# Performance work log

Hardware: AMD Instinct MI355X
Metric: run time of the kernel (lower is better)

## Reference

```python
import jax, jax.numpy as jnp
import numpy as np
from jax.scipy.special import xlogy

LAMBDA_XM = 0.05
LAMBDA_SEG2D = 1.0
BN_EPS = 1e-5


def setup_inputs() -> dict:
    key = jax.random.key(0)
    ks = jax.random.split(key, 40)
    S, N, Nv, B, Np, M, H, C, MID = 2, 240000, 80000, 2, 120000, 30000, 64, 20, 16
    Nimg = B * M
    f = lambda i, shape, s=0.05: jax.random.normal(ks[i], shape, jnp.float32) * s
    inp = {
        'img_feat': f(0, (S, Nimg, H), 1.0),
        'pts_feat': f(1, (S, Nv, H), 1.0),
        'coors_inv': jax.random.randint(ks[2], (S, N), 0, Nv),
        'labels': jax.random.randint(ks[3], (N,), 0, C),
        'img_label': jax.random.randint(ks[4], (Nimg,), 0, C),
        'p2img_idx': jax.random.randint(ks[5], (B, M), 0, Np),
        # multihead 3d classifiers (per scale): Linear(H,128)-ReLU-Linear(128,C)
        'w3a': f(6, (S, H, 128)), 'b3a': jnp.zeros((S, 128)),
        'w3b': f(7, (S, 128, C)), 'b3b': jnp.zeros((S, C)),
        # multihead fuse classifiers
        'wfa': f(8, (S, H, 128)), 'bfa': jnp.zeros((S, 128)),
        'wfb': f(9, (S, 128, C)), 'bfb': jnp.zeros((S, C)),
        # attention: fc1(H->H//4), fc2(H->H//4), fc3(H//2->2), conv1/conv2 (1x1 -> linear) + BN
        'fc1w': f(10, (S, H, MID)), 'fc1b': jnp.zeros((S, MID)),
        'fc2w': f(11, (S, H, MID)), 'fc2b': jnp.zeros((S, MID)),
        'fc3w': f(12, (S, 2 * MID, 2)), 'fc3b': jnp.zeros((S, 2)),
        'c1w': f(13, (S, H, H)), 'c1b': jnp.zeros((S, H)),
        'bn1g': jnp.ones((S, H)), 'bn1b': jnp.zeros((S, H)),
        'c2w': f(14, (S, H, H)), 'c2b': jnp.zeros((S, H)),
        'bn2g': jnp.ones((S, H)), 'bn2b': jnp.zeros((S, H)),
        # final classifier Linear(S*H,128)-ReLU-Linear(128,C)
        'clw1': f(15, (S * H, 128)), 'clb1': jnp.zeros((128,)),
        'clw2': f(16, (128, C)), 'clb2': jnp.zeros((C,)),
    }
    return inp


def _mlp2(x, w1, b1, w2, b2):
    return jax.nn.relu(x @ w1 + b1) @ w2 + b2


def _ce(logits, lab):
    logp = jax.nn.log_softmax(logits, -1)
    return -jnp.take_along_axis(logp, lab[:, None], axis=1).mean()


def _lovasz(probs, lab):
    # lovasz-softmax over all classes, averaged over present classes
    C = probs.shape[1]
    fg = jax.nn.one_hot(lab, C, dtype=probs.dtype)  # [N,C]
    errors = jnp.abs(fg - probs)

    def per_class(err_c, fg_c):
        order = jnp.argsort(-err_c)
        e = err_c[order]
        f = fg_c[order]
        gts = f.sum()
        inter = gts - jnp.cumsum(f)
        union = gts + jnp.cumsum(1.0 - f)
        jac = 1.0 - inter / union
        jac = jnp.concatenate([jac[:1], jac[1:] - jac[:-1]])
        return jnp.dot(e, jac)

    losses = jax.vmap(per_class)(errors.T, fg.T)  # [C]
    present = (fg.sum(0) > 0).astype(probs.dtype)
    return jnp.sum(losses * present) / jnp.maximum(present.sum(), 1.0)


def _seg_loss(logits, lab):
    return _ce(logits, lab) + _lovasz(jax.nn.softmax(logits, -1), lab)


def _convbn_relu(x, cw, cb, g, b):
    # 1x1 Conv1d == per-point linear; BN (training-mode batch stats over points)
    y = x @ cw + cb
    mu = y.mean(0)
    var = y.var(0)
    return jax.nn.relu((y - mu) * jax.lax.rsqrt(var + BN_EPS) * g + b)


def reference(img_feat, pts_feat, coors_inv, labels, img_label, p2img_idx,
              w3a, b3a, w3b, b3b, wfa, bfa, wfb, bfb,
              fc1w, fc1b, fc2w, fc2b, fc3w, fc3b,
              c1w, c1b, bn1g, bn1b, c2w, c2b, bn2g, bn2b,
              clw1, clb1, clw2, clb2):
    S, Nv, H = pts_feat.shape
    C = w3b.shape[-1]
    B, M = p2img_idx.shape
    N = labels.shape[0]
    Np = N // B
    # p2img_mapping: per-batch gather composed to one global gather (batch blocks are contiguous/equal)
    gidx = (jnp.arange(B)[:, None] * Np + p2img_idx).reshape(-1)  # [Nimg]

    loss = jnp.float32(0.0)
    feats = []
    for s in range(S):
        pred3d = _mlp2(pts_feat[s], w3a[s], b3a[s], w3b[s], b3b[s])  # [Nv,C]
        # voxelize_labels: majority vote per voxel (== unique+scatter_max count argmax)
        counts = jnp.zeros((Nv, C), jnp.float32).at[coors_inv[s], labels].add(1.0)
        vox_lab = jnp.argmax(counts, axis=1)  # [Nv]
        # gather voxel feats/preds to image-projected points (fused gather)
        idx = coors_inv[s][gidx]  # [Nimg]
        p = pts_feat[s][idx]      # [Nimg,H] pseudo feats
        pts_pred = pred3d[idx]    # [Nimg,C]
        v = img_feat[s]           # [Nimg,H] valid (image) feats
        # Attention fusion
        w = jax.nn.sigmoid(
            jnp.concatenate([p @ fc1w[s] + fc1b[s], v @ fc2w[s] + fc2b[s]], -1) @ fc3w[s] + fc3b[s])  # [Nimg,2]
        fuse = (_convbn_relu(p, c1w[s], c1b[s], bn1g[s], bn1b[s]) * w[:, 0:1]
                + _convbn_relu(v, c2w[s], c2b[s], bn2g[s], bn2b[s]) * w[:, 1:2])
        feats.append(fuse)
        fuse_pred = _mlp2(fuse, wfa[s], bfa[s], wfb[s], bfb[s])
        loss = loss + _seg_loss(pred3d, vox_lab)
        loss = loss + _seg_loss(fuse_pred, img_label) * LAMBDA_SEG2D / S
        # F.kl_div(log_softmax(pts_pred), softmax(fuse_pred)), reduction='mean' over all elements
        pf = jax.nn.softmax(fuse_pred, -1)
        kl = jnp.mean(xlogy(pf, pf) - pf * jax.nn.log_softmax(pts_pred, -1))
        loss = loss + kl * LAMBDA_XM / S
    img_logits = _mlp2(jnp.concatenate(feats, -1), clw1, clb1, clw2, clb2)
    loss = loss + _seg_loss(img_logits, img_label)
    return loss
```

## Files before the change

kernel.cpp:

```cpp
#include <hip/hip_runtime.h>
#include <stdint.h>

static constexpr int NV   = 80000;
static constexpr int NPT  = 240000;
static constexpr int NIMG = 60000;
static constexpr int Hh   = 64;
static constexpr int Cc   = 20;
static constexpr int NPp  = 120000;
static constexpr int Mm   = 30000;
static constexpr int NB     = 8192;
static constexpr int NCH    = 16;
static constexpr int NBLK_GA  = (NIMG + 63) / 64;
static constexpr int NBLK_MLP = NV / 64;
static constexpr int NBLK_CNT = (NPT + 255) / 256;
static constexpr int NBLK_FILL_NV = (NV + 255) / 256;
static constexpr int NBLK_FILL_NI = (NIMG + 255) / 256;
static constexpr int NBLK_HIST = Cc * NCH;
static constexpr int NBLK_GATH = 2 * NIMG * 8 / 256;
static constexpr int NBLK_P3G  = (2 * NIMG + 255) / 256;
#define BN_EPS 1e-5f

using bf16x8 = __attribute__((ext_vector_type(8))) short;
using f32x4  = __attribute__((ext_vector_type(4))) float;

__device__ __forceinline__ float waveReduce(float v) {
  #pragma unroll
  for (int o = 32; o > 0; o >>= 1) v += __shfl_down(v, o);
  return v;
}
__device__ __forceinline__ short f2bf(float f) {
  uint32_t u = __float_as_uint(f);
  return (short)((u + 0x7FFFu + ((u >> 16) & 1u)) >> 16);
}
__device__ __forceinline__ float bf2f(uint32_t h) { return __uint_as_float(h << 16); }
__device__ __forceinline__ uint32_t pk2(float a, float b) {
  return ((uint32_t)(uint16_t)f2bf(a)) | ((uint32_t)(uint16_t)f2bf(b) << 16);
}

struct PackDesc { const float* src; short* dst; int K, Nr, nt; };
struct PackArgs { PackDesc d[14]; };

__global__ void __launch_bounds__(256)
k_pack_zero(PackArgs pa,
            const float* __restrict__ fc1w, const float* __restrict__ fc1b,
            const float* __restrict__ fc2w, const float* __restrict__ fc2b,
            const float* __restrict__ fc3w, const float* __restrict__ fc3b,
            float* __restrict__ attEffs,
            uint4* __restrict__ zb, int zq,
            const int* __restrict__ ci0, const int* __restrict__ ci1,
            const int* __restrict__ p2img,
            int* __restrict__ idx0, int* __restrict__ idx1,
            const float* __restrict__ pts, uint16_t* __restrict__ pgath) {
  int bid = blockIdx.x;
  if (bid >= 384) {
    int g = (bid - 384) * 256 + threadIdx.x;
    int row = g >> 3, q = g & 7;
    int r = (row >= NIMG) ? row - NIMG : row;
    int s1 = (row >= NIMG) ? 1 : 0;
    const int* ci = s1 ? ci1 : ci0;
    int b = (r >= Mm) ? 1 : 0;
    int id = ci[b * NPp + p2img[r]];
    if (q == 0) { if (s1) idx1[r] = id; else idx0[r] = id; }
    const float* src = pts + (size_t)s1 * NV * 64 + (size_t)id * 64 + q * 8;
    float4 a = *(const float4*)src;
    float4 c = *(const float4*)(src + 4);
    uint4 o;
    o.x = pk2(a.x, a.y); o.y = pk2(a.z, a.w);
    o.z = pk2(c.x, c.y); o.w = pk2(c.z, c.w);
    *(uint4*)(pgath + (size_t)row * 64 + q * 8) = o;
    return;
  }
  if (bid >= 128) {
    const uint4 z = make_uint4(0u, 0u, 0u, 0u);
    int i = (bid - 128) * 256 + threadIdx.x;
    for (; i < zq; i += 256 * 256) zb[i] = z;
    return;
  }
  const int stride = 128 * 256;
  for (int di = 0; di < 14; di++) {
    const float* src = pa.d[di].src;
    short* dst = pa.d[di].dst;
    int K = pa.d[di].K, Nr = pa.d[di].Nr, ntiles = pa.d[di].nt;
    int total = (K / 32) * ntiles * 512;
    for (int idx = bid * 256 + threadIdx.x; idx < total; idx += stride) {
      int j = idx & 7, lane = (idx >> 3) & 63, tile = idx >> 9;
      int nt = tile % ntiles, kt = tile / ntiles;
      int k = kt * 32 + (lane >> 4) * 8 + j;
      int n = nt * 16 + (lane & 15);
      float v = (n < Nr) ? src[(size_t)k * Nr + n] : 0.f;
      dst[idx] = f2bf(v);
    }
  }
  if (bid < 2 && threadIdx.x < 64) {
    int s = bid, t = threadIdx.x;
    const float* f1w = fc1w + s * 64 * 16; const float* f1b = fc1b + s * 16;
    const float* f2w = fc2w + s * 64 * 16; const float* f2b = fc2b + s * 16;
    const float* f3w = fc3w + s * 64;      const float* f3b = fc3b + s * 2;
    float* aE = attEffs + s * 320;
    float p0 = 0.f, p1 = 0.f, v0 = 0.f, v1 = 0.f;
    #pragma unroll
    for (int j = 0; j < 16; j++) {
      p0 = fmaf(f1w[t * 16 + j], f3w[j * 2], p0);
      p1 = fmaf(f1w[t * 16 + j], f3w[j * 2 + 1], p1);
      v0 = fmaf(f2w[t * 16 + j], f3w[(16 + j) * 2], v0);
      v1 = fmaf(f2w[t * 16 + j], f3w[(16 + j) * 2 + 1], v1);
    }
    aE[t * 2] = p0; aE[t * 2 + 1] = p1;
    aE[128 + t * 2] = v0; aE[128 + t * 2 + 1] = v1;
    if (t == 0) {
      float b0 = f3b[0], b1 = f3b[1];
      for (int j = 0; j < 16; j++) {
        b0 += f1b[j] * f3w[j * 2] + f2b[j] * f3w[(16 + j) * 2];
        b1 += f1b[j] * f3w[j * 2 + 1] + f2b[j] * f3w[(16 + j) * 2 + 1];
      }
      aE[256] = b0; aE[257] = b1;
    }
  }
}

__device__ void scanbin_body(const unsigned long long* __restrict__ H64,
                             int n, int call, float* __restrict__ lossesC5,
                             int* __restrict__ gts5, int cls) {
  __shared__ int sWC[4], sWF[4];
  __shared__ float sRedF[4];
  int t = threadIdx.x;
  int lane = t & 63, w = t >> 6;
  const uint4* Hv = (const uint4*)(H64 + (size_t)cls * NB + (size_t)t * 32);
  int locC = 0, locF = 0;
  #pragma unroll
  for (int i = 0; i < 16; i++) {
    uint4 u = Hv[i];
    locF += (int)(u.x + u.z);
    locC += (int)(u.y + u.w);
  }
  int sc = locC, sf = locF;
  #pragma unroll
  for (int o = 1; o < 64; o <<= 1) {
    int a = __shfl_up(sc, o);
    int b = __shfl_up(sf, o);
    if (lane >= o) { sc += a; sf += b; }
  }
  if (lane == 63) { sWC[w] = sc; sWF[w] = sf; }
  __syncthreads();
  int offC = 0, offF = 0, Ftot = 0;
  #pragma unroll
  for (int ww = 0; ww < 4; ww++) {
    int fc = sWF[ww];
    Ftot += fc;
    if (ww < w) { offC += sWC[ww]; offF += fc; }
  }
  int runC = offC + sc - locC;
  int runF = offF + sf - locF;
  float gts = (float)Ftot;
  float contrib = 0.f;
  #pragma unroll
  for (int i = 0; i < 16; i++) {
    uint4 u = Hv[i];
    #pragma unroll
    for (int j = 0; j < 2; j++) {
      int cnt = (int)(j ? u.w : u.y), fgc = (int)(j ? u.z : u.x);
      runC += cnt; runF += fgc;
      if (cnt > 0 && Ftot > 0) {
        float r0 = (float)(n - runC);
        float F0 = (float)(Ftot - runF);
        float r1 = r0 + (float)cnt;
        float F1 = F0 + (float)fgc;
        float emean = __uint_as_float((uint32_t)(t * 32 + i * 2 + j) << 17);
        contrib += emean * (r1 / (gts + r1 - F1) - r0 / (gts + r0 - F0));
      }
    }
  }
  contrib = waveReduce(contrib);
  if (lane == 0) sRedF[w] = contrib;
  __syncthreads();
  if (t == 0) {
    lossesC5[call * 32 + cls] = (Ftot > 0) ? (sRedF[0] + sRedF[1] + sRedF[2] + sRedF[3]) : 0.f;
    gts5[call * 32 + cls] = Ftot;
  }
}

__device__ void tile_loss(const float* __restrict__ sL, int r0, int rows, int n,
                          const int* __restrict__ lab, uint16_t* __restrict__ E,
                          float ceScale, float* __restrict__ lossAcc) {
  int t = threadIdx.x;
  if (t < 64) {
    float total = 0.f;
    int gr = r0 + t;
    if (gr < rows) {
      const float* l = sL + t * 21;
      float m = l[0];
      #pragma unroll
      for (int c = 1; c < Cc; c++) m = fmaxf(m, l[c]);
      float ex[Cc]; float se = 0.f;
      #pragma unroll
      for (int c = 0; c < Cc; c++) { ex[c] = expf(l[c] - m); se += ex[c]; }
      float inv = 1.f / se;
      float lse = logf(se);
      int lb = lab[gr];
      total = -(l[lb] - m - lse) * ceScale;
      #pragma unroll
      for (int c = 0; c < Cc; c++) {
        float prob = ex[c] * inv;
        int fg = (c == lb) ? 1 : 0;
        float err = fg ? (1.f - prob) : prob;
        err = fmaxf(err, 0.f);
        uint32_t key = __float_as_uint(err) >> 17;
        E[(size_t)c * n + gr] = (uint16_t)((key << 1) | (uint32_t)fg);
      }
    }
    total = waveReduce(total);
    if (t == 0) atomicAdd(lossAcc, total);
  }
}

template<int D, bool TO_LDS>
__device__ __forceinline__ void mfma_mlp_core(const short* sXb, short* sH, float* sL,
    int r0, int rows,
    const short* __restrict__ pw1, const float* __restrict__ B1,
    const short* __restrict__ pw2, const float* __restrict__ B2,
    float* __restrict__ Out) {
  constexpr int LDB = D + 8;
  constexpr int KT1 = D / 32;
  const int t = threadIdx.x;
  const int lane = t & 63, w = t >> 6;
  const int m = lane & 15, quad = lane >> 4;
  const int rowA = 16 * w + m;
  bf16x8 a1[KT1];
  #pragma unroll
  for (int kt = 0; kt < KT1; kt++)
    a1[kt] = *(const bf16x8*)(sXb + rowA * LDB + kt * 32 + quad * 8);
  __syncthreads();
  const bf16x8* b1 = (const bf16x8*)pw1;
  #pragma unroll
  for (int nt = 0; nt < 8; nt++) {
    f32x4 c = {0.f, 0.f, 0.f, 0.f};
    #pragma unroll
    for (int kt = 0; kt < KT1; kt++)
      c = __builtin_amdgcn_mfma_f32_16x16x32_bf16(a1[kt], b1[(kt * 8 + nt) * 64 + lane], c, 0, 0, 0);
    int col = nt * 16 + m;
    float bc = B1[col];
    #pragma unroll
    for (int reg = 0; reg < 4; reg++)
      sH[(16 * w + quad * 4 + reg) * 136 + col] = f2bf(fmaxf(c[reg] + bc, 0.f));
  }
  __syncthreads();
  bf16x8 a2[4];
  #pragma unroll
  for (int kt = 0; kt < 4; kt++)
    a2[kt] = *(const bf16x8*)(sH + rowA * 136 + kt * 32 + quad * 8);
  if (TO_LDS) __syncthreads();
  const bf16x8* b2 = (const bf16x8*)pw2;
  #pragma unroll
  for (int nt = 0; nt < 2; nt++) {
    f32x4 c = {0.f, 0.f, 0.f, 0.f};
    #pragma unroll
    for (int kt = 0; kt < 4; kt++)
      c = __builtin_amdgcn_mfma_f32_16x16x32_bf16(a2[kt], b2[(kt * 2 + nt) * 64 + lane], c, 0, 0, 0);
    int col = nt * 16 + m;
    if (col < Cc) {
      float bc = B2[col];
      #pragma unroll
      for (int reg = 0; reg < 4; reg++) {
        int rr = 16 * w + quad * 4 + reg;
        if (TO_LDS) {
          sL[rr * 21 + col] = c[reg] + bc;
        } else {
          int gr = r0 + rr;
          if (gr < rows) Out[(size_t)gr * Cc + col] = c[reg] + bc;
        }
      }
    }
  }
}

__device__ void mlp64_body(int bid0, const float* __restrict__ X,
    const short* __restrict__ pw1, const float* __restrict__ B1,
    const short* __restrict__ pw2, const float* __restrict__ B2,
    float* __restrict__ Out, int rows, char* smem) {
  short* buf = (short*)smem;
  int t = threadIdx.x, r0 = bid0 * 64;
  for (int i = t; i < 1024; i += 256) {
    int r = i >> 4, k4 = (i & 15) * 4;
    int gr = r0 + r;
    float4 v = (gr < rows) ? *(const float4*)(X + (size_t)gr * 64 + k4)
                           : make_float4(0.f, 0.f, 0.f, 0.f);
    uint2 p; p.x = pk2(v.x, v.y); p.y = pk2(v.z, v.w);
    *(uint2*)(buf + r * 72 + k4) = p;
  }
  __syncthreads();
  mfma_mlp_core<64, false>(buf, buf, nullptr, r0, rows, pw1, B1, pw2, B2, Out);
}

__device__ void mlp128_loss_body(int bid0, const uint16_t* __restrict__ Xh,
    const short* __restrict__ pw1, const float* __restrict__ B1,
    const short* __restrict__ pw2, const float* __restrict__ B2,
    const int* __restrict__ lab, uint16_t* __restrict__ E, float ce,
    float* __restrict__ lossAcc, char* smem) {
  short* buf = (short*)smem;
  int t = threadIdx.x, r0 = bid0 * 64;
  for (int i = t; i < 2048; i += 256) {
    int r = i >> 5, k4 = (i & 31) * 4;
    int gr = r0 + r;
    uint2 p = (gr < NIMG) ? *(const uint2*)(Xh + (size_t)gr * 128 + k4) : make_uint2(0u, 0u);
    *(uint2*)(buf + r * 136 + k4) = p;
  }
  __syncthreads();
  mfma_mlp_core<128, true>(buf, buf, (float*)buf, r0, NIMG, pw1, B1, pw2, B2, nullptr);
  __syncthreads();
  tile_loss((float*)buf, r0, NIMG, NIMG, lab, E, ce, lossAcc);
}

__device__ void cnt_body(int bid0, const int* __restrict__ ci, const int* __restrict__ labels,
                         int* __restrict__ counts) {
  int i = bid0 * 256 + threadIdx.x;
  if (i < NPT) atomicAdd(&counts[(size_t)ci[i] * Cc + labels[i]], 1);
}

__device__ void colred_body(int bid0, const float* __restrict__ partials,
                            float* __restrict__ red64) {
  int t = threadIdx.x, j = bid0;
  float v = 0.f;
  for (int b = j; b < NBLK_GA; b += 64) v += partials[(size_t)b * 256 + t];
  red64[j * 256 + t] = v;
}

__device__ void p3gath_body(int bid0, const float* __restrict__ pred3d0,
                            const float* __restrict__ pred3d1,
                            const int* __restrict__ idx0, const int* __restrict__ idx1,
                            float* __restrict__ p3g0, float* __restrict__ p3g1) {
  int row = bid0 * 256 + threadIdx.x;
  if (row >= 2 * NIMG) return;
  int s1 = (row >= NIMG) ? 1 : 0;
  int r = s1 ? row - NIMG : row;
  const float* pred = s1 ? pred3d1 : pred3d0;
  float* dst = (s1 ? p3g1 : p3g0) + (size_t)r * Cc;
  const float* src = pred + (size_t)(s1 ? idx1[r] : idx0[r]) * Cc;
  #pragma unroll
  for (int c = 0; c < Cc; c += 2) {
    uint2 v = *(const uint2*)(src + c);
    *(uint2*)(dst + c) = v;
  }
}

__device__ void fill_body(int bid0, const float* __restrict__ logits,
                          const int* __restrict__ lab, const int* __restrict__ vcnt,
                          int n, uint16_t* __restrict__ E,
                          float ceScale, float* __restrict__ lossAcc,
                          const float* __restrict__ p3g, float klScale) {
  int i = bid0 * 256 + threadIdx.x;
  float total = 0.f;
  if (i < n) {
    int lb;
    if (vcnt) {
      const int* crow = vcnt + (size_t)i * Cc;
      int best = crow[0], arg = 0;
      #pragma unroll
      for (int k = 1; k < Cc; k++) {
        int ck = crow[k];
        if (ck > best) { best = ck; arg = k; }
      }
      lb = arg;
    } else {
      lb = lab[i];
    }
    const float* l = logits + (size_t)i * Cc;
    float m = l[0];
    #pragma unroll
    for (int c = 1; c < Cc; c++) m = fmaxf(m, l[c]);
    float ex[Cc]; float se = 0.f;
    #pragma unroll
    for (int c = 0; c < Cc; c++) { ex[c] = expf(l[c] - m); se += ex[c]; }
    float inv = 1.f / se;
    float lse = logf(se);
    total = -(l[lb] - m - lse) * ceScale;
    #pragma unroll
    for (int c = 0; c < Cc; c++) {
      float prob = ex[c] * inv;
      int fg = (c == lb) ? 1 : 0;
      float err = fg ? (1.f - prob) : prob;
      err = fmaxf(err, 0.f);
      uint32_t key = __float_as_uint(err) >> 17;
      E[(size_t)c * n + i] = (uint16_t)((key << 1) | (uint32_t)fg);
    }
    if (p3g) {
      const float* q = p3g + (size_t)i * Cc;
      float mq = q[0];
      #pragma unroll
      for (int c = 1; c < Cc; c++) mq = fmaxf(mq, q[c]);
      float sq = 0.f;
      #pragma unroll
      for (int c = 0; c < Cc; c++) sq += expf(q[c] - mq);
      float lsq = logf(sq);
      float kl = 0.f;
      #pragma unroll
      for (int c = 0; c < Cc; c++) {
        float lf = l[c] - m - lse;
        float pf = ex[c] * inv;
        float lq = q[c] - mq - lsq;
        kl += pf * (lf - lq);
      }
      total += kl * klScale;
    }
  }
  total = waveReduce(total);
  __shared__ float sh[4];
  int lane = threadIdx.x & 63, w = threadIdx.x >> 6;
  if (lane == 0) sh[w] = total;
  __syncthreads();
  if (threadIdx.x == 0) atomicAdd(lossAcc, sh[0] + sh[1] + sh[2] + sh[3]);
}

__device__ void hist_body(int bid0, const uint16_t* __restrict__ E, int n,
                          unsigned long long* __restrict__ H64, char* smem) {
  uint32_t* lcf = (uint32_t*)smem;
  int t = threadIdx.x;
  int cls = bid0 / NCH, ch = bid0 - cls * NCH;
  int CHsz = (n + NCH - 1) / NCH;
  int i0 = ch * CHsz;
  int i1 = min(n, i0 + CHsz);
  for (int b = t; b < NB; b += 256) lcf[b] = 0u;
  __syncthreads();
  const uint16_t* Ec = E + (size_t)cls * n;
  for (int i = i0 + t; i < i1; i += 256) {
    uint32_t p = Ec[i];
    atomicAdd(&lcf[p >> 1], 0x10000u | (p & 1u));
  }
  __syncthreads();
  unsigned long long* Hc = H64 + (size_t)cls * NB;
  for (int b = t; b < NB; b += 256) {
    uint32_t v = lcf[b];
    if (v)
      atomicAdd(&Hc[b], ((unsigned long long)(v >> 16) << 32) | (v & 0xFFFFu));
  }
}

__device__ void gatt_body(int bid0, const uint16_t* __restrict__ pg,
                          const float* __restrict__ img,
                          const short* __restrict__ pc1, const float* __restrict__ c1b,
                          const short* __restrict__ pc2, const float* __restrict__ c2b,
                          const float* __restrict__ attEff,
                          uint16_t* __restrict__ y1, uint16_t* __restrict__ y2,
                          float* __restrict__ attw, float* __restrict__ partials,
                          char* smem) {
  short* sP = (short*)smem;
  short* sV = (short*)(smem + 9216);
  float* sAtt  = (float*)(smem + 18432);
  float* sStat = (float*)smem;
  int t = threadIdx.x;
  int r0 = bid0 * 64;
  for (int i = t; i < 512; i += 256) {
    int r = i >> 3, q = i & 7;
    int gr = r0 + r;
    uint4 pv = make_uint4(0u, 0u, 0u, 0u);
    if (gr < NIMG) pv = *(const uint4*)(pg + (size_t)gr * 64 + q * 8);
    *(uint4*)(sP + r * 72 + q * 8) = pv;
  }
  for (int i = t; i < 1024; i += 256) {
    int r = i >> 4, q = i & 15;
    int gr = r0 + r;
    float4 vv = make_float4(0.f, 0.f, 0.f, 0.f);
    if (gr < NIMG) vv = *(const float4*)(img + (size_t)gr * 64 + q * 4);
    uint2 qv;
    qv.x = pk2(vv.x, vv.y); qv.y = pk2(vv.z, vv.w);
    *(uint2*)(sV + r * 72 + q * 4) = qv;
  }
  __syncthreads();
  {
    int r = t & 63, qq = t >> 6;
    const float* aP = attEff;
    const float* aV = attEff + 128;
    float l0 = 0.f, l1 = 0.f;
    for (int k = qq * 16; k < qq * 16 + 16; k += 4) {
      uint2 up = *(const uint2*)(sP + r * 72 + k);
      uint2 uv = *(const uint2*)(sV + r * 72 + k);
      float p0 = bf2f(up.x & 0xffff), p1 = bf2f(up.x >> 16);
      float p2 = bf2f(up.y & 0xffff), p3 = bf2f(up.y >> 16);
      float v0 = bf2f(uv.x & 0xffff), v1 = bf2f(uv.x >> 16);
      float v2 = bf2f(uv.y & 0xffff), v3 = bf2f(uv.y >> 16);
      float4 wa = *(const float4*)(aP + 2 * k);
      float4 wb = *(const float4*)(aP + 2 * k + 4);
      l0 += p0 * wa.x + p1 * wa.z + p2 * wb.x + p3 * wb.z;
      l1 += p0 * wa.y + p1 * wa.w + p2 * wb.y + p3 * wb.w;
      float4 ua = *(const float4*)(aV + 2 * k);
      float4 ub = *(const float4*)(aV + 2 * k + 4);
      l0 += v0 * ua.x + v1 * ua.z + v2 * ub.x + v3 * ub.z;
      l1 += v0 * ua.y + v1 * ua.w + v2 * ub.y + v3 * ub.w;
    }
    sAtt[r * 8 + qq * 2] = l0;
    sAtt[r * 8 + qq * 2 + 1] = l1;
  }
  const int lane = t & 63, w = t >> 6;
  const int m = lane & 15, quad = lane >> 4;
  const int rowA = 16 * w + m;
  bf16x8 ap[2], av[2];
  #pragma unroll
  for (int kt = 0; kt < 2; kt++) {
    ap[kt] = *(const bf16x8*)(sP + rowA * 72 + kt * 32 + quad * 8);
    av[kt] = *(const bf16x8*)(sV + rowA * 72 + kt * 32 + quad * 8);
  }
  __syncthreads();
  const bf16x8* b1 = (const bf16x8*)pc1;
  const bf16x8* b2 = (const bf16x8*)pc2;
  #pragma unroll
  for (int nt = 0; nt < 4; nt++) {
    int col = nt * 16 + m;
    f32x4 c1 = {0.f, 0.f, 0.f, 0.f}, c2 = {0.f, 0.f, 0.f, 0.f};
    #pragma unroll
    for (int kt = 0; kt < 2; kt++) {
      c1 = __builtin_amdgcn_mfma_f32_16x16x32_bf16(ap[kt], b1[(kt * 4 + nt) * 64 + lane], c1, 0, 0, 0);
      c2 = __builtin_amdgcn_mfma_f32_16x16x32_bf16(av[kt], b2[(kt * 4 + nt) * 64 + lane], c2, 0, 0, 0);
    }
    float bb1 = c1b[col], bb2 = c2b[col];
    float s1 = 0.f, q1 = 0.f, s2 = 0.f, q2 = 0.f;
    #pragma unroll
    for (int reg = 0; reg < 4; reg++) {
      int gr = r0 + 16 * w + quad * 4 + reg;
      if (gr < NIMG) {
        float v1 = c1[reg] + bb1, v2 = c2[reg] + bb2;
        y1[(size_t)gr * 64 + col] = (uint16_t)f2bf(v1);
        y2[(size_t)gr * 64 + col] = (uint16_t)f2bf(v2);
        s1 += v1; q1 = fmaf(v1, v1, q1);
        s2 += v2; q2 = fmaf(v2, v2, q2);
      }
    }
    s1 += __shfl_down(s1, 32); s1 += __shfl_down(s1, 16);
    q1 += __shfl_down(q1, 32); q1 += __shfl_down(q1, 16);
    s2 += __shfl_down(s2, 32); s2 += __shfl_down(s2, 16);
    q2 += __shfl_down(q2, 32); q2 += __shfl_down(q2, 16);
    if (lane < 16) {
      float* base = sStat + (w * 4 + nt) * 64 + lane;
      base[0]  = s1;
      base[16] = q1;
      base[32] = s2;
      base[48] = q2;
    }
  }
  __syncthreads();
  {
    int kind = t >> 6, col = t & 63;
    int nt = col >> 4, mm = col & 15;
    float v = 0.f;
    #pragma unroll
    for (int ww = 0; ww < 4; ww++)
      v += sStat[(ww * 4 + nt) * 64 + kind * 16 + mm];
    partials[(size_t)bid0 * 256 + kind * 64 + col] = v;
  }
  if (t < 64) {
    int gr = r0 + t;
    if (gr < NIMG) {
      float l0 = attEff[256] + sAtt[t * 8] + sAtt[t * 8 + 2] + sAtt[t * 8 + 4] + sAtt[t * 8 + 6];
      float l1 = attEff[257] + sAtt[t * 8 + 1] + sAtt[t * 8 + 3] + sAtt[t * 8 + 5] + sAtt[t * 8 + 7];
      attw[gr * 2]     = 1.f / (1.f + expf(-l0));
      attw[gr * 2 + 1] = 1.f / (1.f + expf(-l1));
    }
  }
}

__device__ void fusemlp_body(int bid0,
    const uint16_t* __restrict__ y1, const uint16_t* __restrict__ y2,
    const float* __restrict__ attw, const float* __restrict__ red64,
    const float* __restrict__ g1, const float* __restrict__ be1,
    const float* __restrict__ g2, const float* __restrict__ be2,
    uint16_t* __restrict__ feats, int s64,
    const short* __restrict__ pw1, const float* __restrict__ B1,
    const short* __restrict__ pw2, const float* __restrict__ B2,
    float* __restrict__ Out, char* smem) {
  short* buf = (short*)smem;
  float* sBn = (float*)(smem + 17408);
  int t = threadIdx.x, r0 = bid0 * 64;
  float acc = 0.f;
  #pragma unroll 8
  for (int b = 0; b < 64; b++) acc += red64[b * 256 + t];
  float* sSum = (float*)buf;
  sSum[t] = acc;
  __syncthreads();
  if (t < 64) {
    float nn = (float)NIMG;
    float mu1 = sSum[t] / nn;
    float var1 = sSum[64 + t] / nn - mu1 * mu1;
    float a1 = g1[t] / sqrtf(var1 + BN_EPS);
    sBn[t] = a1; sBn[64 + t] = be1[t] - mu1 * a1;
    float mu2 = sSum[128 + t] / nn;
    float var2 = sSum[192 + t] / nn - mu2 * mu2;
    float a2 = g2[t] / sqrtf(var2 + BN_EPS);
    sBn[128 + t] = a2; sBn[192 + t] = be2[t] - mu2 * a2;
  }
  __syncthreads();
  for (int i = t; i < 1024; i += 256) {
    int r = i >> 4, q = i & 15;
    int gr = r0 + r;
    uint2 zp = make_uint2(0u, 0u);
    if (gr < NIMG) {
      float4 a1 = *(const float4*)(sBn + q * 4);
      float4 c1 = *(const float4*)(sBn + 64 + q * 4);
      float4 a2 = *(const float4*)(sBn + 128 + q * 4);
      float4 c2 = *(const float4*)(sBn + 192 + q * 4);
      uint2 u1 = *(const uint2*)(y1 + (size_t)gr * 64 + q * 4);
      uint2 u2 = *(const uint2*)(y2 + (size_t)gr * 64 + q * 4);
      float w0 = attw[gr * 2], w1 = attw[gr * 2 + 1];
      float zx = fmaxf(fmaf(bf2f(u1.x & 0xffff), a1.x, c1.x), 0.f) * w0
               + fmaxf(fmaf(bf2f(u2.x & 0xffff), a2.x, c2.x), 0.f) * w1;
      float zy = fmaxf(fmaf(bf2f(u1.x >> 16),   a1.y, c1.y), 0.f) * w0
               + fmaxf(fmaf(bf2f(u2.x >> 16),   a2.y, c2.y), 0.f) * w1;
      float zz = fmaxf(fmaf(bf2f(u1.y & 0xffff), a1.z, c1.z), 0.f) * w0
               + fmaxf(fmaf(bf2f(u2.y & 0xffff), a2.z, c2.z), 0.f) * w1;
      float zw = fmaxf(fmaf(bf2f(u1.y >> 16),   a1.w, c1.w), 0.f) * w0
               + fmaxf(fmaf(bf2f(u2.y >> 16),   a2.w, c2.w), 0.f) * w1;
      zp.x = pk2(zx, zy); zp.y = pk2(zz, zw);
      *(uint2*)(feats + (size_t)gr * 128 + s64 + q * 4) = zp;
    }
    *(uint2*)(buf + r * 72 + q * 4) = zp;
  }
  __syncthreads();
  mfma_mlp_core<64, false>(buf, buf, nullptr, r0, NIMG, pw1, B1, pw2, B2, Out);
}

__global__ void __launch_bounds__(256)
k_mega2(const float* __restrict__ pf0, const float* __restrict__ pf1,
        const uint16_t* __restrict__ pg0, const uint16_t* __restrict__ pg1,
        const float* __restrict__ if0, const float* __restrict__ if1,
        const short* pc1w0, const short* pc1w1, const short* pc2w0, const short* pc2w1,
        const float* c1b, const float* c2b, const float* attEffs,
        uint16_t* y1a, uint16_t* y2a, uint16_t* y1b, uint16_t* y2b,
        float* attw0, float* attw1, float* partials0, float* partials1,
        const short* pw3a0, const float* b3a, const short* pw3b0, const float* b3b,
        const short* pw3a1, const short* pw3b1,
        float* pred3d0, float* pred3d1,
        const int* __restrict__ ci0, const int* __restrict__ ci1,
        const int* __restrict__ labels,
        int* __restrict__ counts0, int* __restrict__ counts1) {
  __shared__ char smem[20480];
  int bid = blockIdx.x;
  if (bid < NBLK_GA) {
    gatt_body(bid, pg0, if0, pc1w0, c1b, pc2w0, c2b, attEffs,
              y1a, y2a, attw0, partials0, smem);
    return;
  }
  bid -= NBLK_GA;
  if (bid < NBLK_GA) {
    gatt_body(bid, pg1, if1, pc1w1, c1b + 64, pc2w1, c2b + 64, attEffs + 320,
              y1b, y2b, attw1, partials1, smem);
    return;
  }
  bid -= NBLK_GA;
  if (bid < NBLK_MLP) { mlp64_body(bid, pf0, pw3a0, b3a, pw3b0, b3b, pred3d0, NV, smem); return; }
  bid -= NBLK_MLP;
  if (bid < NBLK_MLP) { mlp64_body(bid, pf1, pw3a1, b3a + 128, pw3b1, b3b + Cc, pred3d1, NV, smem); return; }
  bid -= NBLK_MLP;
  if (bid < NBLK_CNT) { cnt_body(bid, ci0, labels, counts0); return; }
  cnt_body(bid - NBLK_CNT, ci1, labels, counts1);
}

__global__ void __launch_bounds__(256)
k_fill_colred(const float* __restrict__ l0, const int* __restrict__ vc0, uint16_t* __restrict__ E0,
              const float* __restrict__ l1, const int* __restrict__ vc1, uint16_t* __restrict__ E1,
              float ce, float* __restrict__ lossAcc,
              const float* partials0, float* red64_0,
              const float* partials1, float* red64_1,
              const int* __restrict__ idx0, const int* __restrict__ idx1,
              float* __restrict__ p3g0, float* __restrict__ p3g1) {
  int bid = blockIdx.x;
  if (bid < NBLK_FILL_NV) {
    fill_body(bid, l0, nullptr, vc0, NV, E0, ce, lossAcc, nullptr, 0.f);
    return;
  }
  bid -= NBLK_FILL_NV;
  if (bid < NBLK_FILL_NV) {
    fill_body(bid, l1, nullptr, vc1, NV, E1, ce, lossAcc, nullptr, 0.f);
    return;
  }
  bid -= NBLK_FILL_NV;
  if (bid < 64) { colred_body(bid, partials0, red64_0); return; }
  bid -= 64;
  if (bid < 64) { colred_body(bid, partials1, red64_1); return; }
  p3gath_body(bid - 64, l0, l1, idx0, idx1, p3g0, p3g1);
}

__global__ void __launch_bounds__(256)
k_fuse2_hist2(const uint16_t* y1a, const uint16_t* y2a, const float* attw0, const float* red64_0,
              const uint16_t* y1b, const uint16_t* y2b, const float* attw1, const float* red64_1,
              const float* bn1g, const float* bn1b, const float* bn2g, const float* bn2b,
              uint16_t* feats,
              const short* pwfa0, const float* bfa, const short* pwfb0, const float* bfb,
              const short* pwfa1, const short* pwfb1,
              float* fusepred0, float* fusepred1,
              const uint16_t* __restrict__ E0, unsigned long long* H0,
              const uint16_t* __restrict__ E1, unsigned long long* H2) {
  __shared__ char smem[32768];
  int bid = blockIdx.x;
  if (bid < NBLK_GA) {
    fusemlp_body(bid, y1a, y2a, attw0, red64_0, bn1g, bn1b, bn2g, bn2b, feats, 0,
                 pwfa0, bfa, pwfb0, bfb, fusepred0, smem);
    return;
  }
  bid -= NBLK_GA;
  if (bid < NBLK_GA) {
    fusemlp_body(bid, y1b, y2b, attw1, red64_1, bn1g + 64, bn1b + 64, bn2g + 64, bn2b + 64,
                 feats, 64, pwfa1, bfa + 128, pwfb1, bfb + Cc, fusepred1, smem);
    return;
  }
  bid -= NBLK_GA;
  if (bid < NBLK_HIST) { hist_body(bid, E0, NV, H0, smem); return; }
  hist_body(bid - NBLK_HIST, E1, NV, H2, smem);
}

__global__ void __launch_bounds__(256)
k_finx2(const uint16_t* __restrict__ feats,
        const short* pcl1, const float* clb1, const short* pcl2, const float* clb2,
        const int* __restrict__ img_label, uint16_t* E2, float ce4, float* lossAcc,
        const float* fusepred0, const float* p3g0, uint16_t* E3,
        const float* fusepred1, const float* p3g1, uint16_t* E4,
        float ce, float kl,
        const unsigned long long* H0, const unsigned long long* H2,
        float* lossesC5, int* gts5) {
  __shared__ char smem[17408];
  int bid = blockIdx.x;
  if (bid < NBLK_GA) {
    mlp128_loss_body(bid, feats, pcl1, clb1, pcl2, clb2, img_label, E2, ce4, lossAcc, smem);
    return;
  }
  bid -= NBLK_GA;
  if (bid < NBLK_FILL_NI) {
    fill_body(bid, fusepred0, img_label, nullptr, NIMG, E3, ce, lossAcc, p3g0, kl);
    return;
  }
  bid -= NBLK_FILL_NI;
  if (bid < NBLK_FILL_NI) {
    fill_body(bid, fusepred1, img_label, nullptr, NIMG, E4, ce, lossAcc, p3g1, kl);
    return;
  }
  bid -= NBLK_FILL_NI;
  if (bid < Cc) { scanbin_body(H0, NV, 0, lossesC5, gts5, bid); return; }
  scanbin_body(H2, NV, 2, lossesC5, gts5, bid - Cc);
}

__global__ void __launch_bounds__(256)
k_hist3(const uint16_t* __restrict__ E3, unsigned long long* H1,
        const uint16_t* __restrict__ E4, unsigned long long* H3,
        const uint16_t* __restrict__ E2, unsigned long long* H4) {
  __shared__ char smem[32768];
  int bid = blockIdx.x;
  if (bid < NBLK_HIST) { hist_body(bid, E3, NIMG, H1, smem); return; }
  bid -= NBLK_HIST;
  if (bid < NBLK_HIST) { hist_body(bid, E4, NIMG, H3, smem); return; }
  hist_body(bid - NBLK_HIST, E2, NIMG, H4, smem);
}

__global__ void __launch_bounds__(256)
k_scan3(const unsigned long long* H1, const unsigned long long* H3,
        const unsigned long long* H4,
        float* lossesC5, int* gts5) {
  int bid = blockIdx.x;
  if (bid < Cc) { scanbin_body(H1, NIMG, 1, lossesC5, gts5, bid); return; }
  bid -= Cc;
  if (bid < Cc) { scanbin_body(H3, NIMG, 3, lossesC5, gts5, bid); return; }
  scanbin_body(H4, NIMG, 4, lossesC5, gts5, bid - Cc);
}

__global__ void k_final(const float* __restrict__ lossAcc,
                        const float* __restrict__ lossesC5, const int* __restrict__ gts5,
                        float* __restrict__ out) {
  const float coefs[5] = {1.0f, 0.5f, 1.0f, 0.5f, 1.0f};
  float loss = lossAcc[0];
  for (int call = 0; call < 5; call++) {
    float s = 0.f; int np = 0;
    for (int c = 0; c < Cc; c++)
      if (gts5[call * 32 + c] > 0) { s += lossesC5[call * 32 + c]; np++; }
    loss += coefs[call] * s / (float)(np > 0 ? np : 1);
  }
  out[0] = loss;
}

extern "C" void kernel_launch(void* const* d_in, const int* in_sizes, int n_in,
                              void* d_out, int out_size, void* d_ws, size_t ws_size,
                              hipStream_t stream) {
  const float* img_feat = (const float*)d_in[0];
  const float* pts_feat = (const float*)d_in[1];
  const int* coors_inv  = (const int*)d_in[2];
  const int* labels     = (const int*)d_in[3];
  const int* img_label  = (const int*)d_in[4];
  const int* p2img      = (const int*)d_in[5];
  const float* w3a = (const float*)d_in[6];
  const float* b3a = (const float*)d_in[7];
  const float* w3b = (const float*)d_in[8];
  const float* b3b = (const float*)d_in[9];
  const float* wfa = (const float*)d_in[10];
  const float* bfa = (const float*)d_in[11];
  const float* wfb = (const float*)d_in[12];
  const float* bfb = (const float*)d_in[13];
  const float* fc1w = (const float*)d_in[14];
  const float* fc1b = (const float*)d_in[15];
  const float* fc2w = (const float*)d_in[16];
  const float* fc2b = (const float*)d_in[17];
  const float* fc3w = (const float*)d_in[18];
  const float* fc3b = (const float*)d_in[19];
  const float* c1w  = (const float*)d_in[20];
  const float* c1b  = (const float*)d_in[21];
  const float* bn1g = (const float*)d_in[22];
  const float* bn1b = (const float*)d_in[23];
  const float* c2w  = (const float*)d_in[24];
  const float* c2b  = (const float*)d_in[25];
  const float* bn2g = (const float*)d_in[26];
  const float* bn2b = (const float*)d_in[27];
  const float* clw1 = (const float*)d_in[28];
  const float* clb1 = (const float*)d_in[29];
  const float* clw2 = (const float*)d_in[30];
  const float* clb2 = (const float*)d_in[31];
  (void)in_sizes; (void)n_in; (void)out_size; (void)ws_size;

  char* ws = (char*)d_ws;
  size_t off = 0;
  auto alloc = [&](size_t bytes) { void* p = ws + off; off += (bytes + 255) & ~(size_t)255; return p; };
  uint16_t* feats = (uint16_t*)alloc((size_t)NIMG * 128 * 2);
  uint16_t* pgath = (uint16_t*)alloc((size_t)2 * NIMG * 64 * 2);
  float* pred3d0 = (float*)alloc((size_t)NV * Cc * 4);
  float* pred3d1 = (float*)alloc((size_t)NV * Cc * 4);
  float* p3g0 = (float*)alloc((size_t)NIMG * Cc * 4);
  float* p3g1 = (float*)alloc((size_t)NIMG * Cc * 4);
  int* idx0 = (int*)alloc((size_t)NIMG * 4);
  int* idx1 = (int*)alloc((size_t)NIMG * 4);
  uint16_t* y1a = (uint16_t*)alloc((size_t)NIMG * Hh * 2);
  uint16_t* y2a = (uint16_t*)alloc((size_t)NIMG * Hh * 2);
  uint16_t* y1b = (uint16_t*)alloc((size_t)NIMG * Hh * 2);
  uint16_t* y2b = (uint16_t*)alloc((size_t)NIMG * Hh * 2);
  uint16_t* E0 = (uint16_t*)alloc((size_t)Cc * NV * 2);
  uint16_t* E1 = (uint16_t*)alloc((size_t)Cc * NV * 2);
  uint16_t* E2 = (uint16_t*)alloc((size_t)Cc * NIMG * 2);
  uint16_t* E3 = (uint16_t*)alloc((size_t)Cc * NIMG * 2);
  uint16_t* E4 = (uint16_t*)alloc((size_t)Cc * NIMG * 2);
  float* partials0 = (float*)alloc((size_t)NBLK_GA * 256 * 4);
  float* partials1 = (float*)alloc((size_t)NBLK_GA * 256 * 4);
  float* red64_0 = (float*)alloc(64 * 256 * 4);
  float* red64_1 = (float*)alloc(64 * 256 * 4);
  float* attw0 = (float*)alloc((size_t)NIMG * 2 * 4);
  float* attw1 = (float*)alloc((size_t)NIMG * 2 * 4);
  float* fusepred0 = (float*)alloc((size_t)NIMG * Cc * 4);
  float* fusepred1 = (float*)alloc((size_t)NIMG * Cc * 4);
  short* pwAll = (short*)alloc(86016 * 2);
  short* pw3a0 = pwAll,          * pw3a1 = pwAll + 8192;
  short* pwfa0 = pwAll + 16384,  * pwfa1 = pwAll + 24576;
  short* pw3b0 = pwAll + 32768,  * pw3b1 = pwAll + 36864;
  short* pwfb0 = pwAll + 40960,  * pwfb1 = pwAll + 45056;
  short* pcl1  = pwAll + 49152;
  short* pcl2  = pwAll + 65536;
  short* pc1w0 = pwAll + 69632,  * pc1w1 = pwAll + 73728;
  short* pc2w0 = pwAll + 77824,  * pc2w1 = pwAll + 81920;
  float* attEffs = (float*)alloc(2 * 320 * 4);
  size_t zsize = 1024 + (size_t)5 * Cc * NB * 8 + (size_t)2 * NV * Cc * 4;
  char* zbase = (char*)alloc(zsize);
  float* lossAcc  = (float*)zbase;
  float* lossesC5 = (float*)zbase + 32;
  int*   gts5     = (int*)((float*)zbase + 192);
  unsigned long long* Hbase = (unsigned long long*)(zbase + 1024);
  auto Hc = [&](int call) { return Hbase + (size_t)call * Cc * NB; };
  int* counts0 = (int*)(zbase + 1024 + (size_t)5 * Cc * NB * 8);
  int* counts1 = counts0 + (size_t)NV * Cc;
  int zq = (int)(zsize / 16);

  const float kl = 0.025f / ((float)NIMG * Cc);
  const float* pf0 = pts_feat;
  const float* pf1 = pts_feat + (size_t)NV * Hh;
  const float* if0 = img_feat;
  const float* if1 = img_feat + (size_t)NIMG * Hh;
  const int* ci0 = coors_inv;
  const int* ci1 = coors_inv + NPT;
  uint16_t* pg0 = pgath;
  uint16_t* pg1 = pgath + (size_t)NIMG * 64;

  PackArgs pa;
  pa.d[0]  = {w3a,        pw3a0, 64, 128, 8};
  pa.d[1]  = {w3a + 8192, pw3a1, 64, 128, 8};
  pa.d[2]  = {wfa,        pwfa0, 64, 128, 8};
  pa.d[3]  = {wfa + 8192, pwfa1, 64, 128, 8};
  pa.d[4]  = {w3b,        pw3b0, 128, 20, 2};
  pa.d[5]  = {w3b + 2560, pw3b1, 128, 20, 2};
  pa.d[6]  = {wfb,        pwfb0, 128, 20, 2};
  pa.d[7]  = {wfb + 2560, pwfb1, 128, 20, 2};
  pa.d[8]  = {clw1,       pcl1, 128, 128, 8};
  pa.d[9]  = {clw2,       pcl2, 128, 20, 2};
  pa.d[10] = {c1w,        pc1w0, 64, 64, 4};
  pa.d[11] = {c1w + 4096, pc1w1, 64, 64, 4};
  pa.d[12] = {c2w,        pc2w0, 64, 64, 4};
  pa.d[13] = {c2w + 4096, pc2w1, 64, 64, 4};
  k_pack_zero<<<384 + NBLK_GATH, 256, 0, stream>>>(
      pa, fc1w, fc1b, fc2w, fc2b, fc3w, fc3b, attEffs,
      (uint4*)zbase, zq, ci0, ci1, p2img, idx0, idx1, pts_feat, pgath);

  k_mega2<<<2 * NBLK_GA + 2 * NBLK_MLP + 2 * NBLK_CNT, 256, 0, stream>>>(
      pf0, pf1, pg0, pg1, if0, if1,
      pc1w0, pc1w1, pc2w0, pc2w1, c1b, c2b, attEffs,
      y1a, y2a, y1b, y2b, attw0, attw1, partials0, partials1,
      pw3a0, b3a, pw3b0, b3b, pw3a1, pw3b1, pred3d0, pred3d1,
      ci0, ci1, labels, counts0, counts1);

  k_fill_colred<<<2 * NBLK_FILL_NV + 128 + NBLK_P3G, 256, 0, stream>>>(
      pred3d0, counts0, E0, pred3d1, counts1, E1, 1.0f / NV, lossAcc,
      partials0, red64_0, partials1, red64_1,
      idx0, idx1, p3g0, p3g1);

  k_fuse2_hist2<<<2 * NBLK_GA + 2 * NBLK_HIST, 256, 0, stream>>>(
      y1a, y2a, attw0, red64_0, y1b, y2b, attw1, red64_1,
      bn1g, bn1b, bn2g, bn2b, feats,
      pwfa0, bfa, pwfb0, bfb, pwfa1, pwfb1, fusepred0, fusepred1,
      E0, Hc(0), E1, Hc(2));

  k_finx2<<<NBLK_GA + 2 * NBLK_FILL_NI + 2 * Cc, 256, 0, stream>>>(
      feats, pcl1, clb1, pcl2, clb2,
      img_label, E2, 1.0f / NIMG, lossAcc,
      fusepred0, p3g0, E3,
      fusepred1, p3g1, E4,
      0.5f / NIMG, kl,
      Hc(0), Hc(2), lossesC5, gts5);

  k_hist3<<<3 * NBLK_HIST, 256, 0, stream>>>(
      E3, Hc(1), E4, Hc(3), E2, Hc(4));

  k_scan3<<<3 * Cc, 256, 0, stream>>>(Hc(1), Hc(3), Hc(4), lossesC5, gts5);

  k_final<<<1, 1, 0, stream>>>(lossAcc, lossesC5, gts5, (float*)d_out);
}
```

Measured before the change: 341.2 us.

## Reschedule voxel fill, histogram and scan stages across fused kernels

Moves the voxel-level error fill out of the colred/gather kernel into the fuse-MLP kernel. The voxel histograms move into the final-classifier kernel, and their bin scans move into the image-histogram kernel. Each lovasz stage for the 3D predictions is pushed one launch later so it shares a grid with independent work and shortens the critical path. The trade-off is changed shared-memory footprints per fused kernel, which can affect occupancy, and more uneven block mixes within each launch.

```diff
diff --git a/kernel.cpp b/kernel.cpp
--- a/kernel.cpp
+++ b/kernel.cpp
@@ -652,41 +652,32 @@
 }
 
 __global__ void __launch_bounds__(256)
-k_fill_colred(const float* __restrict__ l0, const int* __restrict__ vc0, uint16_t* __restrict__ E0,
-              const float* __restrict__ l1, const int* __restrict__ vc1, uint16_t* __restrict__ E1,
-              float ce, float* __restrict__ lossAcc,
-              const float* partials0, float* red64_0,
-              const float* partials1, float* red64_1,
-              const int* __restrict__ idx0, const int* __restrict__ idx1,
-              float* __restrict__ p3g0, float* __restrict__ p3g1) {
+k_colred_p3g(const float* partials0, float* red64_0,
+             const float* partials1, float* red64_1,
+             const float* __restrict__ pred3d0, const float* __restrict__ pred3d1,
+             const int* __restrict__ idx0, const int* __restrict__ idx1,
+             float* __restrict__ p3g0, float* __restrict__ p3g1) {
   int bid = blockIdx.x;
-  if (bid < NBLK_FILL_NV) {
-    fill_body(bid, l0, nullptr, vc0, NV, E0, ce, lossAcc, nullptr, 0.f);
-    return;
-  }
-  bid -= NBLK_FILL_NV;
-  if (bid < NBLK_FILL_NV) {
-    fill_body(bid, l1, nullptr, vc1, NV, E1, ce, lossAcc, nullptr, 0.f);
-    return;
-  }
-  bid -= NBLK_FILL_NV;
   if (bid < 64) { colred_body(bid, partials0, red64_0); return; }
   bid -= 64;
   if (bid < 64) { colred_body(bid, partials1, red64_1); return; }
-  p3gath_body(bid - 64, l0, l1, idx0, idx1, p3g0, p3g1);
+  p3gath_body(bid - 64, pred3d0, pred3d1, idx0, idx1, p3g0, p3g1);
 }
 
 __global__ void __launch_bounds__(256)
-k_fuse2_hist2(const uint16_t* y1a, const uint16_t* y2a, const float* attw0, const float* red64_0,
+k_fuse2_fill2(const uint16_t* y1a, const uint16_t* y2a, const float* attw0, const float* red64_0,
               const uint16_t* y1b, const uint16_t* y2b, const float* attw1, const float* red64_1,
               const float* bn1g, const float* bn1b, const float* bn2g, const float* bn2b,
               uint16_t* feats,
               const short* pwfa0, const float* bfa, const short* pwfb0, const float* bfb,
               const short* pwfa1, const short* pwfb1,
               float* fusepred0, float* fusepred1,
-              const uint16_t* __restrict__ E0, unsigned long long* H0,
-              const uint16_t* __restrict__ E1, unsigned long long* H2) {
-  __shared__ char smem[32768];
+              const float* __restrict__ pred3d0, const int* __restrict__ counts0,
+              uint16_t* __restrict__ E0,
+              const float* __restrict__ pred3d1, const int* __restrict__ counts1,
+              uint16_t* __restrict__ E1,
+              float ceNV, float* lossAcc) {
+  __shared__ char smem[18432];
   int bid = blockIdx.x;
   if (bid < NBLK_GA) {
     fusemlp_body(bid, y1a, y2a, attw0, red64_0, bn1g, bn1b, bn2g, bn2b, feats, 0,
@@ -700,8 +691,11 @@
     return;
   }
   bid -= NBLK_GA;
-  if (bid < NBLK_HIST) { hist_body(bid, E0, NV, H0, smem); return; }
-  hist_body(bid - NBLK_HIST, E1, NV, H2, smem);
+  if (bid < NBLK_FILL_NV) {
+    fill_body(bid, pred3d0, nullptr, counts0, NV, E0, ceNV, lossAcc, nullptr, 0.f);
+    return;
+  }
+  fill_body(bid - NBLK_FILL_NV, pred3d1, nullptr, counts1, NV, E1, ceNV, lossAcc, nullptr, 0.f);
 }
 
 __global__ void __launch_bounds__(256)
@@ -711,9 +705,9 @@
         const float* fusepred0, const float* p3g0, uint16_t* E3,
         const float* fusepred1, const float* p3g1, uint16_t* E4,
         float ce, float kl,
-        const unsigned long long* H0, const unsigned long long* H2,
-        float* lossesC5, int* gts5) {
-  __shared__ char smem[17408];
+        const uint16_t* __restrict__ E0, unsigned long long* H0,
+        const uint16_t* __restrict__ E1, unsigned long long* H2) {
+  __shared__ char smem[32768];
   int bid = blockIdx.x;
   if (bid < NBLK_GA) {
     mlp128_loss_body(bid, feats, pcl1, clb1, pcl2, clb2, img_label, E2, ce4, lossAcc, smem);
@@ -730,20 +724,26 @@
     return;
   }
   bid -= NBLK_FILL_NI;
-  if (bid < Cc) { scanbin_body(H0, NV, 0, lossesC5, gts5, bid); return; }
-  scanbin_body(H2, NV, 2, lossesC5, gts5, bid - Cc);
+  if (bid < NBLK_HIST) { hist_body(bid, E0, NV, H0, smem); return; }
+  hist_body(bid - NBLK_HIST, E1, NV, H2, smem);
 }
 
 __global__ void __launch_bounds__(256)
-k_hist3(const uint16_t* __restrict__ E3, unsigned long long* H1,
-        const uint16_t* __restrict__ E4, unsigned long long* H3,
-        const uint16_t* __restrict__ E2, unsigned long long* H4) {
+k_hist3_scan2(const uint16_t* __restrict__ E3, unsigned long long* H1,
+              const uint16_t* __restrict__ E4, unsigned long long* H3,
+              const uint16_t* __restrict__ E2, unsigned long long* H4,
+              const unsigned long long* H0, const unsigned long long* H2s,
+              float* lossesC5, int* gts5) {
   __shared__ char smem[32768];
   int bid = blockIdx.x;
   if (bid < NBLK_HIST) { hist_body(bid, E3, NIMG, H1, smem); return; }
   bid -= NBLK_HIST;
   if (bid < NBLK_HIST) { hist_body(bid, E4, NIMG, H3, smem); return; }
-  hist_body(bid - NBLK_HIST, E2, NIMG, H4, smem);
+  bid -= NBLK_HIST;
+  if (bid < NBLK_HIST) { hist_body(bid, E2, NIMG, H4, smem); return; }
+  bid -= NBLK_HIST;
+  if (bid < Cc) { scanbin_body(H0, NV, 0, lossesC5, gts5, bid); return; }
+  scanbin_body(H2s, NV, 2, lossesC5, gts5, bid - Cc);
 }
 
 __global__ void __launch_bounds__(256)
@@ -893,28 +893,29 @@
       pw3a0, b3a, pw3b0, b3b, pw3a1, pw3b1, pred3d0, pred3d1,
       ci0, ci1, labels, counts0, counts1);
 
-  k_fill_colred<<<2 * NBLK_FILL_NV + 128 + NBLK_P3G, 256, 0, stream>>>(
-      pred3d0, counts0, E0, pred3d1, counts1, E1, 1.0f / NV, lossAcc,
+  k_colred_p3g<<<128 + NBLK_P3G, 256, 0, stream>>>(
       partials0, red64_0, partials1, red64_1,
-      idx0, idx1, p3g0, p3g1);
-
-  k_fuse2_hist2<<<2 * NBLK_GA + 2 * NBLK_HIST, 256, 0, stream>>>(
+      pred3d0, pred3d1, idx0, idx1, p3g0, p3g1);
+
+  k_fuse2_fill2<<<2 * NBLK_GA + 2 * NBLK_FILL_NV, 256, 0, stream>>>(
       y1a, y2a, attw0, red64_0, y1b, y2b, attw1, red64_1,
       bn1g, bn1b, bn2g, bn2b, feats,
       pwfa0, bfa, pwfb0, bfb, pwfa1, pwfb1, fusepred0, fusepred1,
-      E0, Hc(0), E1, Hc(2));
-
-  k_finx2<<<NBLK_GA + 2 * NBLK_FILL_NI + 2 * Cc, 256, 0, stream>>>(
+      pred3d0, counts0, E0, pred3d1, counts1, E1,
+      1.0f / NV, lossAcc);
+
+  k_finx2<<<NBLK_GA + 2 * NBLK_FILL_NI + 2 * NBLK_HIST, 256, 0, stream>>>(
       feats, pcl1, clb1, pcl2, clb2,
       img_label, E2, 1.0f / NIMG, lossAcc,
       fusepred0, p3g0, E3,
       fusepred1, p3g1, E4,
       0.5f / NIMG, kl,
+      E0, Hc(0), E1, Hc(2));
+
+  k_hist3_scan2<<<3 * NBLK_HIST + 2 * Cc, 256, 0, stream>>>(
+      E3, Hc(1), E4, Hc(3), E2, Hc(4),
       Hc(0), Hc(2), lossesC5, gts5);
 
-  k_hist3<<<3 * NBLK_HIST, 256, 0, stream>>>(
-      E3, Hc(1), E4, Hc(3), E2, Hc(4));
-
   k_scan3<<<3 * Cc, 256, 0, stream>>>(Hc(1), Hc(3), Hc(4), lossesC5, gts5);
 
   k_final<<<1, 1, 0, stream>>>(lossAcc, lossesC5, gts5, (float*)d_out);
```

After: 339.0 us. Within noise of the previous version (-0.6%).
